# Kernel optimization log

Hardware: AMD Instinct MI355X
Metric: run time of the kernel (lower is better)

Reference implementation:

```python
import jax, jax.numpy as jnp
import numpy as np

B, S, D_IN, D_OUT = 4, 2048, 2048, 2048
E, R, TOP_K = 8, 8, 2
ALPHA = 16.0
SCALE = ALPHA / R  # alpha / r


def setup_inputs() -> dict:
    key = jax.random.key(0)
    ks = jax.random.split(key, 6)
    x = jax.random.normal(ks[0], (B, S, D_IN), dtype=jnp.float32)
    # base frozen linear: torch Linear weight [out, in], bias [out]
    W_base = jax.random.normal(ks[1], (D_OUT, D_IN), dtype=jnp.float32) / np.sqrt(D_IN)
    b_base = jax.random.normal(ks[2], (D_OUT,), dtype=jnp.float32) * 0.01
    # router: Linear(in_features, num_experts, bias=False) -> weight [E, in]
    W_router = jax.random.normal(ks[3], (E, D_IN), dtype=jnp.float32) / np.sqrt(D_IN)
    # LoRA experts: A [E, r, in], B [E, out, r] (torch inits B to zero; use small
    # random values so outputs/grads are non-trivial -- math is identical)
    A_w = jax.random.normal(ks[4], (E, R, D_IN), dtype=jnp.float32) / np.sqrt(D_IN)
    B_w = jax.random.normal(ks[5], (E, D_OUT, R), dtype=jnp.float32) * 0.02
    return {"x": x, "W_base": W_base, "b_base": b_base,
            "W_router": W_router, "A_w": A_w, "B_w": B_w}


def reference(x, W_base, b_base, W_router, A_w, B_w):
    # frozen base linear: [B,S,out]
    y = jnp.einsum('bsd,od->bso', x, W_base) + b_base
    # router: logits [B,S,E] -> top-k + softmax over the k selected logits
    logits = jnp.einsum('bsd,ed->bse', x, W_router)
    topk_vals, topk_idx = jax.lax.top_k(logits, TOP_K)       # [B,S,k]
    gates = jax.nn.softmax(topk_vals, axis=-1)               # [B,S,k]
    # all-experts LoRA compute (matches the original dense-stack semantics)
    h = jnp.einsum('bsd,erd->bser', x, A_w)                  # [B,S,E,r]
    expert_outs = jnp.einsum('bser,eor->bseo', h, B_w) * SCALE  # [B,S,E,out]
    # gather the top-k expert outputs and combine with gates
    topk_outs = jnp.take_along_axis(expert_outs, topk_idx[..., None], axis=2)  # [B,S,k,out]
    fused = jnp.sum(topk_outs * gates[..., None], axis=2)    # [B,S,out]
    return y + fused
```

## Files before the change

kernel.cpp:

```cpp
#include <hip/hip_runtime.h>

typedef unsigned short u16;
typedef __attribute__((ext_vector_type(8))) short short8;
typedef __attribute__((ext_vector_type(4))) float f32x4;

#define GLL16(g, l) __builtin_amdgcn_global_load_lds(                         \
    (const __attribute__((address_space(1))) void*)(g),                        \
    (__attribute__((address_space(3))) void*)(l), 16, 0, 0)

__device__ __forceinline__ u16 f2bf(float f) {
  union { float f; unsigned u; } v; v.f = f;
  unsigned u = v.u;
  return (u16)((u + 0x7FFFu + ((u >> 16) & 1u)) >> 16);
}

__device__ __forceinline__ float bf2f(u16 u) {
  union { unsigned u; float f; } v; v.u = ((unsigned)u) << 16;
  return v.f;
}

__device__ __forceinline__ ushort4 cvt4(float4 v) {
  ushort4 o; o.x = f2bf(v.x); o.y = f2bf(v.y); o.z = f2bf(v.z); o.w = f2bf(v.w);
  return o;
}

__global__ __launch_bounds__(512) void k_pre(
    const float* __restrict__ x, const float* __restrict__ Wr,
    const float* __restrict__ Wb, const float* __restrict__ Aw,
    const float* __restrict__ Bw,
    u16* __restrict__ xbf, float* __restrict__ logits,
    u16* __restrict__ wbf, u16* __restrict__ aabf, u16* __restrict__ bmt)
{
  __shared__ float wlds[16384];
  {
    const float4* src = (const float4*)Wr;
    float4* dst = (float4*)wlds;
    int t = threadIdx.x;
#pragma unroll
    for (int i = 0; i < 8; ++i) dst[t + i * 512] = src[t + i * 512];
  }
  __syncthreads();
  const int wave = threadIdx.x >> 6, lane = threadIdx.x & 63;
  const float4* wv = (const float4*)wlds;
#pragma unroll 1
  for (int s = 0; s < 2; ++s) {
    int tok = blockIdx.x * 16 + wave * 2 + s;
    const float4* xrow = (const float4*)(x + tok * 2048);
    ushort4* orow = (ushort4*)(xbf + tok * 2048);
    float acc[8];
#pragma unroll
    for (int e = 0; e < 8; ++e) acc[e] = 0.f;
#pragma unroll 1
    for (int i = 0; i < 8; ++i) {
      float4 xv = xrow[lane + i * 64];
      orow[lane + i * 64] = cvt4(xv);
#pragma unroll
      for (int e = 0; e < 8; ++e) {
        float4 b = wv[e * 512 + lane + i * 64];
        acc[e] += xv.x * b.x + xv.y * b.y + xv.z * b.z + xv.w * b.w;
      }
    }
#pragma unroll
    for (int e = 0; e < 8; ++e) {
      float v = acc[e];
#pragma unroll
      for (int off = 32; off > 0; off >>= 1) v += __shfl_xor(v, off, 64);
      acc[e] = v;
    }
    if (lane == 0) {
#pragma unroll
      for (int e = 0; e < 8; ++e) logits[tok * 8 + e] = acc[e];
    }
  }
  const int tidg = blockIdx.x * 512 + threadIdx.x;
  {
    const float4* src = (const float4*)Wb;
    ushort4* dst = (ushort4*)wbf;
#pragma unroll
    for (int i = 0; i < 4; ++i)
      dst[tidg + i * 262144] = cvt4(src[tidg + i * 262144]);
  }
  if (tidg < 32768) {
    ((ushort4*)aabf)[tidg] = cvt4(((const float4*)Aw)[tidg]);
  }
  if (tidg < 2048) {
    const int n = tidg;
#pragma unroll
    for (int e = 0; e < 8; ++e) {
      const float4* src = (const float4*)(Bw + e * 16384 + n * 8);
      ushort4* dst = (ushort4*)(bmt + n * 64 + e * 8);
      dst[0] = cvt4(src[0]);
      dst[1] = cvt4(src[1]);
    }
  }
}

__global__ __launch_bounds__(256) void k_hgemm(
    const u16* __restrict__ xbf, const u16* __restrict__ aabf,
    u16* __restrict__ P)
{
  __shared__ u16 As[256 * 64];
  __shared__ u16 Bs[64 * 64];
  int t = threadIdx.x, wave = t >> 6, lane = t & 63;
  int mBase = blockIdx.x * 256;
  int ks = blockIdx.y;
  int fr = lane & 15, fg = lane >> 4;
  int lrow = lane >> 3, lcol = (lane & 7) * 8;
  f32x4 zero = {0.f, 0.f, 0.f, 0.f};
  f32x4 acc[4][4];
#pragma unroll
  for (int i = 0; i < 4; ++i)
#pragma unroll
    for (int j = 0; j < 4; ++j) acc[i][j] = zero;
#pragma unroll 1
  for (int it = 0; it < 4; ++it) {
    int k0 = ks * 256 + it * 64;
    __syncthreads();
#pragma unroll
    for (int cc = 0; cc < 8; ++cc) {
      int c = wave * 8 + cc;
      GLL16(xbf + (mBase + c * 8 + lrow) * 2048 + k0 + lcol, &As[c * 512]);
    }
#pragma unroll
    for (int cc = 0; cc < 2; ++cc) {
      int c = wave * 2 + cc;
      GLL16(aabf + (c * 8 + lrow) * 2048 + k0 + lcol, &Bs[c * 512]);
    }
    __syncthreads();
#pragma unroll
    for (int kk = 0; kk < 2; ++kk) {
      short8 a[4], bfr[4];
#pragma unroll
      for (int i = 0; i < 4; ++i)
        a[i] = *(const short8*)&As[(wave * 64 + i * 16 + fr) * 64 + kk * 32 + fg * 8];
#pragma unroll
      for (int j = 0; j < 4; ++j)
        bfr[j] = *(const short8*)&Bs[(j * 16 + fr) * 64 + kk * 32 + fg * 8];
#pragma unroll
      for (int i = 0; i < 4; ++i)
#pragma unroll
        for (int j = 0; j < 4; ++j)
          acc[i][j] = __builtin_amdgcn_mfma_f32_16x16x32_bf16(a[i], bfr[j], acc[i][j], 0, 0, 0);
    }
  }
#pragma unroll
  for (int i = 0; i < 4; ++i)
#pragma unroll
    for (int j = 0; j < 4; ++j)
#pragma unroll
      for (int r = 0; r < 4; ++r) {
        int m = mBase + wave * 64 + i * 16 + fg * 4 + r;
        int n = j * 16 + fr;
        P[(ks * 8192 + m) * 64 + n] = f2bf(acc[i][j][r]);
      }
}

__global__ __launch_bounds__(256) void k_topk(
    const float* __restrict__ logits, const u16* __restrict__ P,
    u16* __restrict__ G)
{
  int t = threadIdx.x, wave = t >> 6, lane = t & 63;
  int tok = blockIdx.x * 4 + wave;
  const float* lg = logits + tok * 8;
  float la[8];
#pragma unroll
  for (int e = 0; e < 8; ++e) la[e] = lg[e];
  float v0 = la[0]; int i0 = 0;
#pragma unroll
  for (int e = 1; e < 8; ++e) { if (la[e] > v0) { v0 = la[e]; i0 = e; } }
  float v1 = -3.4e38f; int i1 = 0;
#pragma unroll
  for (int e = 0; e < 8; ++e) { if (e != i0 && la[e] > v1) { v1 = la[e]; i1 = e; } }
  float ex = expf(v1 - v0);
  float inv = 1.f / (1.f + ex);
  float gate0 = inv, gate1 = ex * inv;
  int e = lane >> 3;
  float h = 0.f;
#pragma unroll
  for (int ks = 0; ks < 8; ++ks) h += bf2f(P[(ks * 8192 + tok) * 64 + lane]);
  float g = (e == i0) ? gate0 : ((e == i1) ? gate1 : 0.f);
  G[tok * 64 + lane] = f2bf(2.0f * g * h);
}

__global__ __launch_bounds__(256, 3) void k_main(
    const u16* __restrict__ xbf, const u16* __restrict__ wbf,
    const u16* __restrict__ G, const u16* __restrict__ BmT,
    const float* __restrict__ bias, float* __restrict__ out)
{
  __shared__ u16 lds[24576];
  const int tid = threadIdx.x;
  const int w = tid >> 6, lane = tid & 63;
  const int fr = lane & 15, fg = lane >> 4;
  const int wr = w >> 1, wc = w & 1;

  const int b0 = blockIdx.x;
  const int xcd = b0 & 7, ii = b0 >> 3;
  const int mBase = (xcd * 8 + (ii >> 4)) * 128;
  const int nBase = (ii & 15) * 128;

  const int rl = lane >> 3;
  const int ce = ((lane & 7) ^ rl) << 3;
  const int swz = (fr & 7) << 3;
  const int colk0 = (fg * 8) ^ swz;
  const int colk1 = (32 + fg * 8) ^ swz;
  const int aOff = (wr * 64 + fr) * 64;
  const int bOff = (wc * 64 + fr) * 64;

  const u16* pA = xbf + (mBase + w * 32 + rl) * 2048 + ce;
  const u16* pB = wbf + (nBase + w * 32 + rl) * 2048 + ce;

  f32x4 acc[4][4];
  const f32x4 zero = {0.f, 0.f, 0.f, 0.f};
#pragma unroll
  for (int mi = 0; mi < 4; ++mi)
#pragma unroll
    for (int nj = 0; nj < 4; ++nj) acc[mi][nj] = zero;

  short8 a[4][2];
  short8 U[2][2], V[2][2];

#define LGKM(N) asm volatile("s_waitcnt lgkmcnt(" #N ")" ::: "memory")
#define VMC(N)  asm volatile("s_waitcnt vmcnt(" #N ")" ::: "memory")
#define BAR()   __builtin_amdgcn_s_barrier()

#define SA() { GLL16(pA,         lds + w * 2048);                             \
               GLL16(pA + 16384, lds + w * 2048 + 512);                       \
               GLL16(pA + 32768, lds + w * 2048 + 1024);                      \
               GLL16(pA + 49152, lds + w * 2048 + 1536);                      \
               pA += 64; }
#define SB(BOFF) { GLL16(pB,         lds + (BOFF) + w * 2048);                \
                   GLL16(pB + 16384, lds + (BOFF) + w * 2048 + 512);          \
                   GLL16(pB + 32768, lds + (BOFF) + w * 2048 + 1024);         \
                   GLL16(pB + 49152, lds + (BOFF) + w * 2048 + 1536);         \
                   pB += 64; }

#define RDA()                                                                 \
  _Pragma("unroll")                                                           \
  for (int mi = 0; mi < 4; ++mi) {                                            \
    a[mi][0] = *(const short8*)(lds + aOff + mi * 1024 + colk0);              \
    a[mi][1] = *(const short8*)(lds + aOff + mi * 1024 + colk1);              \
  }

#define RDB2(DST, BOFF, NJ0)                                                  \
  DST[0][0] = *(const short8*)(lds + (BOFF) + bOff + (NJ0) * 1024 + colk0);   \
  DST[0][1] = *(const short8*)(lds + (BOFF) + bOff + (NJ0) * 1024 + colk1);   \
  DST[1][0] = *(const short8*)(lds + (BOFF) + bOff + ((NJ0)+1) * 1024 + colk0);\
  DST[1][1] = *(const short8*)(lds + (BOFF) + bOff + ((NJ0)+1) * 1024 + colk1);

#define MFMAP(BV, NJ0)                                                        \
  __builtin_amdgcn_s_setprio(1);                                              \
  _Pragma("unroll")                                                           \
  for (int kk = 0; kk < 2; ++kk)                                              \
    _Pragma("unroll")                                                         \
    for (int mi = 0; mi < 4; ++mi)                                            \
      _Pragma("unroll")                                                       \
      for (int j = 0; j < 2; ++j)                                             \
        acc[mi][(NJ0) + j] = __builtin_amdgcn_mfma_f32_16x16x32_bf16(         \
            a[mi][kk], BV[j][kk], acc[mi][(NJ0) + j], 0, 0, 0);               \
  __builtin_amdgcn_s_setprio(0);

#define TILE(BCUR, SBS, SAS)                                                  \
  {                                                                           \
                                                                      \
    VMC(0);                                                                   \
    BAR();                                                                    \
    RDB2(U, BCUR, 0)                                                          \
    RDA()                                                                     \
    RDB2(V, BCUR, 2)                                                          \
    LGKM(4);                                                                  \
    MFMAP(U, 0)                                                               \
    BAR();                                                                    \
                                                                      \
    SAS                                                                       \
    SBS                                                                       \
    LGKM(0);                                                                  \
    MFMAP(V, 2)                                                               \
  }

  SA()
  SB(8192)

#pragma unroll 1
  for (int tt = 0; tt < 15; ++tt) {
    TILE(8192, SB(16384), SA())
    TILE(16384, SB(8192), SA())
  }
  TILE(8192, SB(16384), SA())
  {
    const u16* pG = G + (mBase + w * 32 + rl) * 64 + ce;
    const u16* pT = BmT + (nBase + w * 32 + rl) * 64 + ce;
    TILE(16384,
         { GLL16(pT,        lds + 8192 + w * 2048);
           GLL16(pT + 512,  lds + 8192 + w * 2048 + 512);
           GLL16(pT + 1024, lds + 8192 + w * 2048 + 1024);
           GLL16(pT + 1536, lds + 8192 + w * 2048 + 1536); },
         { GLL16(pG,        lds + w * 2048);
           GLL16(pG + 512,  lds + w * 2048 + 512);
           GLL16(pG + 1024, lds + w * 2048 + 1024);
           GLL16(pG + 1536, lds + w * 2048 + 1536); })
  }
  TILE(8192, {}, {})

#pragma unroll
  for (int nj = 0; nj < 4; ++nj) {
    const int n = nBase + wc * 64 + nj * 16 + fr;
    const float bv = bias[n];
#pragma unroll
    for (int mi = 0; mi < 4; ++mi) {
      const int m = mBase + wr * 64 + mi * 16 + fg * 4;
#pragma unroll
      for (int r = 0; r < 4; ++r)
        out[(m + r) * 2048 + n] = acc[mi][nj][r] + bv;
    }
  }
#undef TILE
#undef MFMAP
#undef RDB2
#undef RDA
#undef SB
#undef SA
#undef BAR
#undef VMC
#undef LGKM
}

extern "C" void kernel_launch(void* const* d_in, const int* in_sizes, int n_in,
                              void* d_out, int out_size, void* d_ws, size_t ws_size,
                              hipStream_t stream) {
  const float* x  = (const float*)d_in[0];
  const float* Wb = (const float*)d_in[1];
  const float* bb = (const float*)d_in[2];
  const float* Wr = (const float*)d_in[3];
  const float* Aw = (const float*)d_in[4];
  const float* Bw = (const float*)d_in[5];

  char* ws = (char*)d_ws;
  u16*   xbf  = (u16*)  (ws + 0);
  u16*   wbf  = (u16*)  (ws + 33554432);
  u16*   aabf = (u16*)  (ws + 41943040);
  u16*   bmt  = (u16*)  (ws + 42205184);
  float* lgt  = (float*)(ws + 42467328);
  u16*   G    = (u16*)  (ws + 42729472);
  u16*   P   = (u16*)d_out;
  float* out = (float*)d_out;

  hipLaunchKernelGGL(k_pre,   dim3(512),   dim3(512), 0, stream,
                     x, Wr, Wb, Aw, Bw, xbf, lgt, wbf, aabf, bmt);
  hipLaunchKernelGGL(k_hgemm, dim3(32, 8), dim3(256), 0, stream, xbf, aabf, P);
  hipLaunchKernelGGL(k_topk,  dim3(2048),  dim3(256), 0, stream, lgt, P, G);
  hipLaunchKernelGGL(k_main,  dim3(1024),  dim3(256), 0, stream,
                     xbf, wbf, G, bmt, bb, out);
}
```

Measured before the change: 121.1 us.

## Use 256x128 tiles with W pre-packed in MFMA fragment layout loaded to registers

The main GEMM block tile grows from 128x128 to 256x128, halving the grid and doubling per-block reuse of the base weight. The weight and LoRA-B matrices are now pre-packed in the pre-pass into MFMA fragment order, so each wave loads B operands straight from global memory into registers instead of staging them through LDS. Only the activation tile goes through LDS, with double buffering. This cuts LDS traffic and global re-reads of W, at the cost of higher register pressure (occupancy drops from 3 to 2 blocks per CU) and exposing global load latency on the B path.

```diff
diff --git a/kernel.cpp b/kernel.cpp
--- a/kernel.cpp
+++ b/kernel.cpp
@@ -29,7 +29,7 @@
     const float* __restrict__ Wb, const float* __restrict__ Aw,
     const float* __restrict__ Bw,
     u16* __restrict__ xbf, float* __restrict__ logits,
-    u16* __restrict__ wbf, u16* __restrict__ aabf, u16* __restrict__ bmt)
+    u16* __restrict__ wpk, u16* __restrict__ aabf, u16* __restrict__ bpk)
 {
   __shared__ float wlds[16384];
   {
@@ -73,12 +73,19 @@
     }
   }
   const int tidg = blockIdx.x * 512 + threadIdx.x;
-  {
-    const float4* src = (const float4*)Wb;
-    ushort4* dst = (ushort4*)wbf;
-#pragma unroll
-    for (int i = 0; i < 4; ++i)
-      dst[tidg + i * 262144] = cvt4(src[tidg + i * 262144]);
+  if (tidg < 131072) {
+    const int k8 = tidg & 255;
+    const int n4 = tidg >> 8;
+    const int n0 = n4 * 4, k = k8 * 8;
+    const int wbase = ((n0 >> 4) * 64 + (k >> 5)) * 512 +
+                      (((k >> 3) & 3) * 16 + (n0 & 15)) * 8;
+#pragma unroll
+    for (int r = 0; r < 4; ++r) {
+      const float4* s = (const float4*)(Wb + (n0 + r) * 2048 + k);
+      ushort4* d = (ushort4*)(wpk + wbase + r * 8);
+      d[0] = cvt4(s[0]);
+      d[1] = cvt4(s[1]);
+    }
   }
   if (tidg < 32768) {
     ((ushort4*)aabf)[tidg] = cvt4(((const float4*)Aw)[tidg]);
@@ -88,7 +95,8 @@
 #pragma unroll
     for (int e = 0; e < 8; ++e) {
       const float4* src = (const float4*)(Bw + e * 16384 + n * 8);
-      ushort4* dst = (ushort4*)(bmt + n * 64 + e * 8);
+      ushort4* dst = (ushort4*)(bpk + ((n >> 4) * 2 + (e >> 2)) * 512 +
+                                ((e & 3) * 16 + (n & 15)) * 8);
       dst[0] = cvt4(src[0]);
       dst[1] = cvt4(src[1]);
     }
@@ -182,12 +190,12 @@
   G[tok * 64 + lane] = f2bf(2.0f * g * h);
 }
 
-__global__ __launch_bounds__(256, 3) void k_main(
-    const u16* __restrict__ xbf, const u16* __restrict__ wbf,
-    const u16* __restrict__ G, const u16* __restrict__ BmT,
+__global__ __launch_bounds__(256, 2) void k_main(
+    const u16* __restrict__ xbf, const u16* __restrict__ wpk,
+    const u16* __restrict__ G, const u16* __restrict__ bpk,
     const float* __restrict__ bias, float* __restrict__ out)
 {
-  __shared__ u16 lds[24576];
+  __shared__ u16 lds[32768];
   const int tid = threadIdx.x;
   const int w = tid >> 6, lane = tid & 63;
   const int fr = lane & 15, fg = lane >> 4;
@@ -195,7 +203,7 @@
 
   const int b0 = blockIdx.x;
   const int xcd = b0 & 7, ii = b0 >> 3;
-  const int mBase = (xcd * 8 + (ii >> 4)) * 128;
+  const int mBase = (xcd * 4 + (ii >> 4)) * 256;
   const int nBase = (ii & 15) * 128;
 
   const int rl = lane >> 3;
@@ -203,121 +211,159 @@
   const int swz = (fr & 7) << 3;
   const int colk0 = (fg * 8) ^ swz;
   const int colk1 = (32 + fg * 8) ^ swz;
-  const int aOff = (wr * 64 + fr) * 64;
-  const int bOff = (wc * 64 + fr) * 64;
-
-  const u16* pA = xbf + (mBase + w * 32 + rl) * 2048 + ce;
-  const u16* pB = wbf + (nBase + w * 32 + rl) * 2048 + ce;
-
-  f32x4 acc[4][4];
+  const int aOff = (wr * 128 + fr) * 64;
+
+  const u16* pA = xbf + (mBase + w * 8 + rl) * 2048 + ce;
+  const u16* pW = wpk + (((nBase >> 4) + wc * 4) * 64) * 512 + lane * 8;
+
+  f32x4 acc[8][4];
   const f32x4 zero = {0.f, 0.f, 0.f, 0.f};
 #pragma unroll
-  for (int mi = 0; mi < 4; ++mi)
+  for (int mi = 0; mi < 8; ++mi)
 #pragma unroll
     for (int nj = 0; nj < 4; ++nj) acc[mi][nj] = zero;
 
-  short8 a[4][2];
-  short8 U[2][2], V[2][2];
+  short8 aE[2][2], aO[2][2];
+  short8 Bt[4][2], Bn[4][2];
 
 #define LGKM(N) asm volatile("s_waitcnt lgkmcnt(" #N ")" ::: "memory")
 #define VMC(N)  asm volatile("s_waitcnt vmcnt(" #N ")" ::: "memory")
 #define BAR()   __builtin_amdgcn_s_barrier()
 
-#define SA() { GLL16(pA,         lds + w * 2048);                             \
-               GLL16(pA + 16384, lds + w * 2048 + 512);                       \
-               GLL16(pA + 32768, lds + w * 2048 + 1024);                      \
-               GLL16(pA + 49152, lds + w * 2048 + 1536);                      \
-               pA += 64; }
-#define SB(BOFF) { GLL16(pB,         lds + (BOFF) + w * 2048);                \
-                   GLL16(pB + 16384, lds + (BOFF) + w * 2048 + 512);          \
-                   GLL16(pB + 32768, lds + (BOFF) + w * 2048 + 1024);         \
-                   GLL16(pB + 49152, lds + (BOFF) + w * 2048 + 1536);         \
-                   pB += 64; }
-
-#define RDA()                                                                 \
-  _Pragma("unroll")                                                           \
-  for (int mi = 0; mi < 4; ++mi) {                                            \
-    a[mi][0] = *(const short8*)(lds + aOff + mi * 1024 + colk0);              \
-    a[mi][1] = *(const short8*)(lds + aOff + mi * 1024 + colk1);              \
-  }
-
-#define RDB2(DST, BOFF, NJ0)                                                  \
-  DST[0][0] = *(const short8*)(lds + (BOFF) + bOff + (NJ0) * 1024 + colk0);   \
-  DST[0][1] = *(const short8*)(lds + (BOFF) + bOff + (NJ0) * 1024 + colk1);   \
-  DST[1][0] = *(const short8*)(lds + (BOFF) + bOff + ((NJ0)+1) * 1024 + colk0);\
-  DST[1][1] = *(const short8*)(lds + (BOFF) + bOff + ((NJ0)+1) * 1024 + colk1);
-
-#define MFMAP(BV, NJ0)                                                        \
+#define SA(DOFF) {                                                            \
+    GLL16(pA,           lds + (DOFF) + w * 512);                              \
+    GLL16(pA + 65536,   lds + (DOFF) + 2048 + w * 512);                       \
+    GLL16(pA + 131072,  lds + (DOFF) + 4096 + w * 512);                       \
+    GLL16(pA + 196608,  lds + (DOFF) + 6144 + w * 512);                       \
+    GLL16(pA + 262144,  lds + (DOFF) + 8192 + w * 512);                       \
+    GLL16(pA + 327680,  lds + (DOFF) + 10240 + w * 512);                      \
+    GLL16(pA + 393216,  lds + (DOFF) + 12288 + w * 512);                      \
+    GLL16(pA + 458752,  lds + (DOFF) + 14336 + w * 512);                      \
+    pA += 64; }
+
+#define LB0(BN_) {                                                            \
+    BN_[0][0] = *(const short8*)(pW);                                         \
+    BN_[0][1] = *(const short8*)(pW + 512);                                   \
+    BN_[1][0] = *(const short8*)(pW + 32768);                                 \
+    BN_[1][1] = *(const short8*)(pW + 32768 + 512); }
+#define LB1(BN_) {                                                            \
+    BN_[2][0] = *(const short8*)(pW + 65536);                                 \
+    BN_[2][1] = *(const short8*)(pW + 65536 + 512);                           \
+    BN_[3][0] = *(const short8*)(pW + 98304);                                 \
+    BN_[3][1] = *(const short8*)(pW + 98304 + 512);                           \
+    pW += 1024; }
+
+#define RDA2(DST, POFF, MI0)                                                  \
+  DST[0][0] = *(const short8*)(lds + (POFF) + aOff + (MI0) * 1024 + colk0);   \
+  DST[0][1] = *(const short8*)(lds + (POFF) + aOff + (MI0) * 1024 + colk1);   \
+  DST[1][0] = *(const short8*)(lds + (POFF) + aOff + ((MI0)+1) * 1024 + colk0);\
+  DST[1][1] = *(const short8*)(lds + (POFF) + aOff + ((MI0)+1) * 1024 + colk1);
+
+#define MFMAQ(AV, BV, MI0)                                                    \
   __builtin_amdgcn_s_setprio(1);                                              \
   _Pragma("unroll")                                                           \
   for (int kk = 0; kk < 2; ++kk)                                              \
     _Pragma("unroll")                                                         \
-    for (int mi = 0; mi < 4; ++mi)                                            \
+    for (int q = 0; q < 2; ++q)                                               \
       _Pragma("unroll")                                                       \
-      for (int j = 0; j < 2; ++j)                                             \
-        acc[mi][(NJ0) + j] = __builtin_amdgcn_mfma_f32_16x16x32_bf16(         \
-            a[mi][kk], BV[j][kk], acc[mi][(NJ0) + j], 0, 0, 0);               \
+      for (int nj = 0; nj < 4; ++nj)                                          \
+        acc[(MI0) + q][nj] = __builtin_amdgcn_mfma_f32_16x16x32_bf16(         \
+            AV[q][kk], BV[nj][kk], acc[(MI0) + q][nj], 0, 0, 0);              \
   __builtin_amdgcn_s_setprio(0);
 
-#define TILE(BCUR, SBS, SAS)                                                  \
+#define TILE(POFF, BC, BN_, SAS, LB0S, LB1S)                                  \
   {                                                                           \
                                                                       \
+    VMC(8);                                                                   \
+    BAR();                                                                    \
+    RDA2(aE, POFF, 0)                                                         \
+    LGKM(0);                                                                  \
     VMC(0);                                                                   \
-    BAR();                                                                    \
-    RDB2(U, BCUR, 0)                                                          \
-    RDA()                                                                     \
-    RDB2(V, BCUR, 2)                                                          \
-    LGKM(4);                                                                  \
-    MFMAP(U, 0)                                                               \
-    BAR();                                                                    \
+    MFMAQ(aE, BC, 0)                                                          \
                                                                       \
     SAS                                                                       \
-    SBS                                                                       \
+    RDA2(aO, POFF, 2)                                                         \
     LGKM(0);                                                                  \
-    MFMAP(V, 2)                                                               \
-  }
-
-  SA()
-  SB(8192)
+    MFMAQ(aO, BC, 2)                                                          \
+                                                                      \
+    LB0S                                                                      \
+    RDA2(aE, POFF, 4)                                                         \
+    LGKM(0);                                                                  \
+    MFMAQ(aE, BC, 4)                                                          \
+                                                                      \
+    LB1S                                                                      \
+    RDA2(aO, POFF, 6)                                                         \
+    LGKM(0);                                                                  \
+    MFMAQ(aO, BC, 6)                                                          \
+  }
+
+  SA(0)
+  LB0(Bt) LB1(Bt)
+  VMC(8);
+  BAR();
 
 #pragma unroll 1
   for (int tt = 0; tt < 15; ++tt) {
-    TILE(8192, SB(16384), SA())
-    TILE(16384, SB(8192), SA())
-  }
-  TILE(8192, SB(16384), SA())
+    TILE(0, Bt, Bn, SA(16384), LB0(Bn), LB1(Bn))
+    TILE(16384, Bn, Bt, SA(0), LB0(Bt), LB1(Bt))
+  }
+  TILE(0, Bt, Bn, SA(16384), LB0(Bn), LB1(Bn))
   {
-    const u16* pG = G + (mBase + w * 32 + rl) * 64 + ce;
-    const u16* pT = BmT + (nBase + w * 32 + rl) * 64 + ce;
-    TILE(16384,
-         { GLL16(pT,        lds + 8192 + w * 2048);
-           GLL16(pT + 512,  lds + 8192 + w * 2048 + 512);
-           GLL16(pT + 1024, lds + 8192 + w * 2048 + 1024);
-           GLL16(pT + 1536, lds + 8192 + w * 2048 + 1536); },
-         { GLL16(pG,        lds + w * 2048);
-           GLL16(pG + 512,  lds + w * 2048 + 512);
-           GLL16(pG + 1024, lds + w * 2048 + 1024);
-           GLL16(pG + 1536, lds + w * 2048 + 1536); })
-  }
-  TILE(8192, {}, {})
+    const u16* pG = G + (mBase + w * 8 + rl) * 64 + ce;
+    const u16* pL = bpk + ((nBase >> 4) + wc * 4) * 1024 + lane * 8;
+    TILE(16384, Bn, Bt,
+         { GLL16(pG,         lds + w * 512);
+           GLL16(pG + 2048,  lds + 2048 + w * 512);
+           GLL16(pG + 4096,  lds + 4096 + w * 512);
+           GLL16(pG + 6144,  lds + 6144 + w * 512);
+           GLL16(pG + 8192,  lds + 8192 + w * 512);
+           GLL16(pG + 10240, lds + 10240 + w * 512);
+           GLL16(pG + 12288, lds + 12288 + w * 512);
+           GLL16(pG + 14336, lds + 14336 + w * 512); },
+         { Bt[0][0] = *(const short8*)(pL);
+           Bt[0][1] = *(const short8*)(pL + 512);
+           Bt[1][0] = *(const short8*)(pL + 1024);
+           Bt[1][1] = *(const short8*)(pL + 1536); },
+         { Bt[2][0] = *(const short8*)(pL + 2048);
+           Bt[2][1] = *(const short8*)(pL + 2560);
+           Bt[3][0] = *(const short8*)(pL + 3072);
+           Bt[3][1] = *(const short8*)(pL + 3584); })
+  }
+  {
+    VMC(8);
+    BAR();
+    RDA2(aE, 0, 0)
+    LGKM(0);
+    VMC(0);
+    MFMAQ(aE, Bt, 0)
+    RDA2(aO, 0, 2)
+    LGKM(0);
+    MFMAQ(aO, Bt, 2)
+    RDA2(aE, 0, 4)
+    LGKM(0);
+    MFMAQ(aE, Bt, 4)
+    RDA2(aO, 0, 6)
+    LGKM(0);
+    MFMAQ(aO, Bt, 6)
+  }
 
 #pragma unroll
   for (int nj = 0; nj < 4; ++nj) {
     const int n = nBase + wc * 64 + nj * 16 + fr;
     const float bv = bias[n];
 #pragma unroll
-    for (int mi = 0; mi < 4; ++mi) {
-      const int m = mBase + wr * 64 + mi * 16 + fg * 4;
+    for (int mi = 0; mi < 8; ++mi) {
+      const int m = mBase + wr * 128 + mi * 16 + fg * 4;
 #pragma unroll
       for (int r = 0; r < 4; ++r)
         out[(m + r) * 2048 + n] = acc[mi][nj][r] + bv;
     }
   }
 #undef TILE
-#undef MFMAP
-#undef RDB2
-#undef RDA
-#undef SB
+#undef MFMAQ
+#undef RDA2
+#undef LB1
+#undef LB0
 #undef SA
 #undef BAR
 #undef VMC
@@ -336,18 +382,18 @@
 
   char* ws = (char*)d_ws;
   u16*   xbf  = (u16*)  (ws + 0);
-  u16*   wbf  = (u16*)  (ws + 33554432);
+  u16*   wpk  = (u16*)  (ws + 33554432);
   u16*   aabf = (u16*)  (ws + 41943040);
-  u16*   bmt  = (u16*)  (ws + 42205184);
+  u16*   bpk  = (u16*)  (ws + 42205184);
   float* lgt  = (float*)(ws + 42467328);
   u16*   G    = (u16*)  (ws + 42729472);
   u16*   P   = (u16*)d_out;
   float* out = (float*)d_out;
 
   hipLaunchKernelGGL(k_pre,   dim3(512),   dim3(512), 0, stream,
-                     x, Wr, Wb, Aw, Bw, xbf, lgt, wbf, aabf, bmt);
+                     x, Wr, Wb, Aw, Bw, xbf, lgt, wpk, aabf, bpk);
   hipLaunchKernelGGL(k_hgemm, dim3(32, 8), dim3(256), 0, stream, xbf, aabf, P);
   hipLaunchKernelGGL(k_topk,  dim3(2048),  dim3(256), 0, stream, lgt, P, G);
-  hipLaunchKernelGGL(k_main,  dim3(1024),  dim3(256), 0, stream,
-                     xbf, wbf, G, bmt, bb, out);
-}
+  hipLaunchKernelGGL(k_main,  dim3(512),   dim3(256), 0, stream,
+                     xbf, wpk, G, bpk, bb, out);
+}
```

Result: faster. 108.7 us (-10.2%).
